# Kernel tuning notes

Hardware: AMD Instinct MI355X
Metric: run time of the kernel (lower is better)

Reference implementation:

```python
import jax, jax.numpy as jnp
import numpy as np

H = 16      # attention_head_num
DH = 64     # attention_head_size
D = H * DH  # out_dim = 1024


def setup_inputs() -> dict:
    key = jax.random.key(0)
    ks = jax.random.split(key, 9)
    s = 1.0 / np.sqrt(D)
    x = jax.random.normal(ks[0], (2, 2048, D), dtype=jnp.float32)
    Wq = jax.random.uniform(ks[1], (D, D), jnp.float32, -s, s)
    bq = jax.random.uniform(ks[2], (D,), jnp.float32, -s, s)
    Wk = jax.random.uniform(ks[3], (D, D), jnp.float32, -s, s)
    bk = jax.random.uniform(ks[4], (D,), jnp.float32, -s, s)
    Wv = jax.random.uniform(ks[5], (D, D), jnp.float32, -s, s)
    bv = jax.random.uniform(ks[6], (D,), jnp.float32, -s, s)
    Wo = jax.random.uniform(ks[7], (D, D), jnp.float32, -s, s)
    bo = jax.random.uniform(ks[8], (D,), jnp.float32, -s, s)
    return {"x": x, "Wq": Wq, "bq": bq, "Wk": Wk, "bk": bk,
            "Wv": Wv, "bv": bv, "Wo": Wo, "bo": bo}


def reference(x, Wq, bq, Wk, bk, Wv, bv, Wo, bo):
    B, S, _ = x.shape
    # projections (nn.Linear: x @ W^T + b)
    q = (x @ Wq.T + bq).reshape(B, S, H, DH).transpose(0, 2, 1, 3)  # [B,H,S,Dh]
    k = (x @ Wk.T + bk).reshape(B, S, H, DH).transpose(0, 2, 1, 3)
    v = (x @ Wv.T + bv).reshape(B, S, H, DH).transpose(0, 2, 1, 3)
    scores = jnp.einsum('bhqd,bhkd->bhqk', q, k) / jnp.sqrt(jnp.float32(DH))
    probs = jax.nn.softmax(scores, axis=-1)  # dropout is identity in eval mode
    ctx = jnp.einsum('bhqk,bhkd->bhqd', probs, v)
    ctx = ctx.transpose(0, 2, 1, 3).reshape(B, S, D)
    return ctx @ Wo.T + bo
```

## Files before the change

### kernel.cpp

```cpp
#include <hip/hip_runtime.h>
#include <hip/hip_bf16.h>
#include <stdint.h>

typedef __attribute__((ext_vector_type(8))) short bf16x8;
typedef __attribute__((ext_vector_type(8))) unsigned short u16x8;
typedef __attribute__((ext_vector_type(4))) unsigned short u16x4;
typedef __attribute__((ext_vector_type(4))) float f32x4;

constexpr int NB  = 2;
constexpr int NS  = 2048;
constexpr int NH  = 16;
constexpr int NDH = 64;
constexpr int ND  = 1024;

static __device__ __forceinline__ unsigned short bfbits(float f) {
    union { float f; uint32_t u; } v; v.f = f;
    uint32_t u = v.u + 0x7FFFu + ((v.u >> 16) & 1u);
    return (unsigned short)(u >> 16);
}

static __device__ __forceinline__ float fexp2(float x) {
#if __has_builtin(__builtin_amdgcn_exp2f)
    return __builtin_amdgcn_exp2f(x);
#else
    return exp2f(x);
#endif
}

static __device__ __forceinline__ void gl_lds16(const void* g, void* l) {
    __builtin_amdgcn_global_load_lds(
        (const __attribute__((address_space(1))) unsigned int*)g,
        (__attribute__((address_space(3))) unsigned int*)l, 16, 0, 0);
}

__global__ __launch_bounds__(256)
void cvt_kernel(const float* __restrict__ x,  const float* __restrict__ wq,
                const float* __restrict__ wk, const float* __restrict__ wv,
                const float* __restrict__ wo,
                unsigned short* __restrict__ xb,  unsigned short* __restrict__ wqb,
                unsigned short* __restrict__ wkb, unsigned short* __restrict__ wvb,
                unsigned short* __restrict__ wob)
{
    const int b = blockIdx.x;
    const float* s; unsigned short* d; int off;
    if      (b < 2048) { s = x;  d = xb;  off = b; }
    else if (b < 2560) { s = wq; d = wqb; off = b - 2048; }
    else if (b < 3072) { s = wk; d = wkb; off = b - 2560; }
    else if (b < 3584) { s = wv; d = wvb; off = b - 3072; }
    else               { s = wo; d = wob; off = b - 3584; }
    const size_t idx = ((size_t)off * 256 + threadIdx.x) * 8;
    float4 f0 = *(const float4*)&s[idx];
    float4 f1 = *(const float4*)&s[idx + 4];
    u16x8 o;
    o[0] = bfbits(f0.x); o[1] = bfbits(f0.y); o[2] = bfbits(f0.z); o[3] = bfbits(f0.w);
    o[4] = bfbits(f1.x); o[5] = bfbits(f1.y); o[6] = bfbits(f1.z); o[7] = bfbits(f1.w);
    *(u16x8*)&d[idx] = o;
}

__global__ __launch_bounds__(256, 2)
void qkv_kernel(const unsigned short* __restrict__ xb,
                const unsigned short* __restrict__ wqb,
                const unsigned short* __restrict__ wkb,
                const unsigned short* __restrict__ wvb,
                const float* __restrict__ bq, const float* __restrict__ bk,
                const float* __restrict__ bv,
                unsigned short* __restrict__ qbuf,
                unsigned short* __restrict__ kbuf,
                unsigned short* __restrict__ vtbuf)
{
    __shared__ unsigned short As[128 * 64];
    __shared__ unsigned short Bs[128 * 64];
    __shared__ unsigned short Tt[128][136];

    const int fid = blockIdx.x + blockIdx.y * 24;
    const int xcd = fid & 7, idx = fid >> 3;
    const int bx  = idx >> 2;
    const int by  = xcd * 4 + (idx & 3);

    const int m0  = by * 128;
    const int jg0 = bx * 128;
    const int proj = jg0 >> 10;
    const int n0   = jg0 & 1023;
    const unsigned short* W = (proj == 0) ? wqb : (proj == 1) ? wkb : wvb;
    const float* bias       = (proj == 0) ? bq  : (proj == 1) ? bk  : bv;

    const int tid = threadIdx.x, lane = tid & 63, wid = tid >> 6;
    const int wm = wid >> 1, wn = wid & 1;
    const int l15 = lane & 15, g = lane >> 4;

    const f32x4 fzero = {0.f, 0.f, 0.f, 0.f};
    f32x4 acc[4][4];
#pragma unroll
    for (int i = 0; i < 4; i++)
#pragma unroll
        for (int j = 0; j < 4; j++) acc[i][j] = fzero;

    const int srow = tid >> 3;
    const int scb  = ((tid & 7) * 16) ^ ((srow & 7) << 4);
    const char* asrc = (const char*)xb + (size_t)(m0 + srow) * 2048 + scb;
    const char* bsrc = (const char*)W  + (size_t)(n0 + srow) * 2048 + scb;
    char* adst = (char*)As + tid * 16;
    char* bdst = (char*)Bs + tid * 16;
    const int xm = (l15 & 7) << 4;

    for (int k0 = 0; k0 < 1024; k0 += 64) {
#pragma unroll
        for (int i = 0; i < 4; i++) {
            gl_lds16(asrc + (size_t)i * 32 * 2048 + k0 * 2, adst + i * 4096);
            gl_lds16(bsrc + (size_t)i * 32 * 2048 + k0 * 2, bdst + i * 4096);
        }
        __syncthreads();
#pragma unroll
        for (int kk = 0; kk < 2; kk++) {
            bf16x8 af[4], bfr[4];
#pragma unroll
            for (int i = 0; i < 4; i++) {
                const int row = wm * 64 + i * 16 + l15;
                af[i] = *(const bf16x8*)((const char*)As + row * 128 + ((kk * 64 + g * 16) ^ xm));
            }
#pragma unroll
            for (int j = 0; j < 4; j++) {
                const int row = wn * 64 + j * 16 + l15;
                bfr[j] = *(const bf16x8*)((const char*)Bs + row * 128 + ((kk * 64 + g * 16) ^ xm));
            }
#pragma unroll
            for (int i = 0; i < 4; i++)
#pragma unroll
                for (int j = 0; j < 4; j++)
                    acc[i][j] = __builtin_amdgcn_mfma_f32_16x16x32_bf16(af[i], bfr[j], acc[i][j], 0, 0, 0);
        }
        __syncthreads();
    }

    if (proj < 2) {
        unsigned short* qk_out = (proj == 0) ? qbuf : kbuf;
        const float qs = (proj == 0) ? 0.18033688f : 1.0f;
#pragma unroll
        for (int j = 0; j < 4; j++) {
            const int col = n0 + wn * 64 + j * 16 + l15;
            const float bsv = bias[col];
            const int h = col >> 6, dh = col & 63;
#pragma unroll
            for (int i = 0; i < 4; i++)
#pragma unroll
                for (int r = 0; r < 4; r++) {
                    const int row = m0 + wm * 64 + i * 16 + g * 4 + r;
                    const int b_ = row >> 11, s_ = row & (NS - 1);
                    qk_out[((size_t)((b_ * NH + h) * NS + s_)) * NDH + dh] =
                        bfbits((acc[i][j][r] + bsv) * qs);
                }
        }
    } else {
#pragma unroll
        for (int j = 0; j < 4; j++) {
            const int cl = wn * 64 + j * 16 + l15;
            const float bsv = bias[n0 + cl];
#pragma unroll
            for (int i = 0; i < 4; i++) {
                u16x4 w4;
#pragma unroll
                for (int r = 0; r < 4; r++) w4[r] = bfbits(acc[i][j][r] + bsv);
                *(u16x4*)&Tt[cl][wm * 64 + i * 16 + g * 4] = w4;
            }
        }
        __syncthreads();
        const int b_ = m0 >> 11, s0 = m0 & (NS - 1);
        const int h0 = n0 >> 6;
#pragma unroll
        for (int it = 0; it < 8; it++) {
            const int c = wid * 32 + it * 4 + g;
            u16x8 v8 = *(const u16x8*)&Tt[c][l15 * 8];
            const size_t row = (size_t)(b_ * NH + h0 + (c >> 6)) * NDH + (c & 63);
            *(u16x8*)&vtbuf[row * NS + s0 + l15 * 8] = v8;
        }
    }
}

__global__ __launch_bounds__(512, 6)
void attn_kernel(const unsigned short* __restrict__ qbuf,
                 const unsigned short* __restrict__ kbuf,
                 const unsigned short* __restrict__ vtbuf,
                 unsigned short* __restrict__ ctxbuf)
{
    __shared__ unsigned short Ks[3][64 * 64];
    __shared__ unsigned short Vs[3][64 * 64];

    const int fid  = blockIdx.x + blockIdx.y * 16;
    const int nid  = (fid % 8) * 64 + fid / 8;
    const int bx   = nid % 16, bh = nid / 16;
    const int q0   = bx * 128;

    const int tid = threadIdx.x, lane = tid & 63, wid = tid >> 6;
    const int l15 = lane & 15, g = lane >> 4;

    const unsigned short* qb = qbuf  + (size_t)bh * NS * NDH;
    const unsigned short* kb = kbuf  + (size_t)bh * NS * NDH;
    const unsigned short* vb = vtbuf + (size_t)bh * NDH * NS;

    const int qrow = q0 + wid * 16 + l15;
    const bf16x8 qf0 = *(const bf16x8*)&qb[(size_t)qrow * NDH + g * 8];
    const bf16x8 qf1 = *(const bf16x8*)&qb[(size_t)qrow * NDH + 32 + g * 8];

    const short oneb = (short)0x3F80;
    const bf16x8 ones = {oneb, oneb, oneb, oneb, oneb, oneb, oneb, oneb};

    const f32x4 fzero = {0.f, 0.f, 0.f, 0.f};
    f32x4 acc[4];
#pragma unroll
    for (int d = 0; d < 4; d++) acc[d] = fzero;
    f32x4 acc_l = fzero;

    const int o = tid * 16;
    const int srow = o >> 7;
    const int scb  = (o & 127) ^ ((srow & 7) << 4);
    const char* ksrc = (const char*)kb + srow * 128 + scb;
    const char* vsrc = (const char*)vb + (size_t)srow * (NS * 2) + scb;
    char* kbase = (char*)Ks;
    char* vbase = (char*)Vs;
    const int xm = (l15 & 7) << 4;

    auto STAGE = [&](int b, int t_) {
        gl_lds16(ksrc + (size_t)t_ * 8192, kbase + b * 8192 + o);
        gl_lds16(vsrc + (size_t)t_ * 128,  vbase + b * 8192 + o);
    };

    STAGE(0, 0);
    STAGE(1, 1);

    for (int t = 0; t < 32; t++) {
        if (t < 31) asm volatile("s_waitcnt vmcnt(2)" ::: "memory");
        else        asm volatile("s_waitcnt vmcnt(0)" ::: "memory");
        __builtin_amdgcn_s_barrier();
        asm volatile("" ::: "memory");
        if (t < 30) STAGE((t + 2) % 3, t + 2);

        const char* ksb = kbase + (t % 3) * 8192;
        const char* vsb = vbase + (t % 3) * 8192;

        f32x4 sv[4];
        __builtin_amdgcn_s_setprio(1);
#pragma unroll
        for (int kt = 0; kt < 4; kt++) {
            const char* rb = ksb + (kt * 16 + l15) * 128;
            bf16x8 kf0 = *(const bf16x8*)(rb + ((g * 16) ^ xm));
            bf16x8 kf1 = *(const bf16x8*)(rb + ((64 + g * 16) ^ xm));
            f32x4 s4 = fzero;
            s4 = __builtin_amdgcn_mfma_f32_16x16x32_bf16(kf0, qf0, s4, 0, 0, 0);
            s4 = __builtin_amdgcn_mfma_f32_16x16x32_bf16(kf1, qf1, s4, 0, 0, 0);
            sv[kt] = s4;
        }
        __builtin_amdgcn_s_setprio(0);

#pragma unroll
        for (int kt = 0; kt < 4; kt++)
#pragma unroll
            for (int r = 0; r < 4; r++)
                sv[kt][r] = fexp2(sv[kt][r]);

        bf16x8 pf[2];
#pragma unroll
        for (int f = 0; f < 2; f++) {
            const int kt0 = f * 2;
            union { __hip_bfloat162 h2; uint32_t u; } c0, c1, c2, c3;
            float2 p01 = { sv[kt0][0], sv[kt0][1] };
            float2 p23 = { sv[kt0][2], sv[kt0][3] };
            float2 p45 = { sv[kt0 + 1][0], sv[kt0 + 1][1] };
            float2 p67 = { sv[kt0 + 1][2], sv[kt0 + 1][3] };
            c0.h2 = __float22bfloat162_rn(p01);
            c1.h2 = __float22bfloat162_rn(p23);
            c2.h2 = __float22bfloat162_rn(p45);
            c3.h2 = __float22bfloat162_rn(p67);
            uint32_t a0 = c0.u, a1 = c1.u, b0 = c2.u, b1 = c3.u;
            asm("v_permlane32_swap_b32 %0, %1" : "+v"(a0), "+v"(b0));
            asm("v_permlane32_swap_b32 %0, %1" : "+v"(a1), "+v"(b1));
            asm("v_permlane16_swap_b32 %0, %1" : "+v"(a0), "+v"(b0));
            asm("v_permlane16_swap_b32 %0, %1" : "+v"(a1), "+v"(b1));
            union { uint32_t w[4]; bf16x8 fr; } r_;
            r_.w[0] = a0; r_.w[1] = a1; r_.w[2] = b0; r_.w[3] = b1;
            pf[f] = r_.fr;
        }

        __builtin_amdgcn_s_setprio(1);
        acc_l = __builtin_amdgcn_mfma_f32_16x16x32_bf16(pf[0], ones, acc_l, 0, 0, 0);
        acc_l = __builtin_amdgcn_mfma_f32_16x16x32_bf16(pf[1], ones, acc_l, 0, 0, 0);
#pragma unroll
        for (int d = 0; d < 4; d++) {
            const char* rb = vsb + (d * 16 + l15) * 128;
            bf16x8 vf0 = *(const bf16x8*)(rb + ((g * 16) ^ xm));
            bf16x8 vf1 = *(const bf16x8*)(rb + ((64 + g * 16) ^ xm));
            acc[d] = __builtin_amdgcn_mfma_f32_16x16x32_bf16(pf[0], vf0, acc[d], 0, 0, 0);
            acc[d] = __builtin_amdgcn_mfma_f32_16x16x32_bf16(pf[1], vf1, acc[d], 0, 0, 0);
        }
        __builtin_amdgcn_s_setprio(0);
    }

    const int b_ = bh >> 4, h_ = bh & 15;
#pragma unroll
    for (int r = 0; r < 4; r++) {
        const float inv = 1.f / acc_l[r];
        const int sq = q0 + wid * 16 + g * 4 + r;
        const size_t base = ((size_t)(b_ * NS + sq)) * ND + h_ * NDH;
#pragma unroll
        for (int d = 0; d < 4; d++)
            ctxbuf[base + d * 16 + l15] = bfbits(acc[d][r] * inv);
    }
}

__global__ __launch_bounds__(256, 2)
void out_kernel(const unsigned short* __restrict__ ctx,
                const unsigned short* __restrict__ wob,
                const float* __restrict__ bo,
                float* __restrict__ out)
{
    __shared__ unsigned short As[128 * 64];
    __shared__ unsigned short Bs[128 * 64];

    const int n0 = blockIdx.x * 128;
    const int m0 = blockIdx.y * 128;
    const int tid = threadIdx.x, lane = tid & 63, wid = tid >> 6;
    const int wm = wid >> 1, wn = wid & 1;
    const int l15 = lane & 15, g = lane >> 4;

    const f32x4 fzero = {0.f, 0.f, 0.f, 0.f};
    f32x4 acc[4][4];
#pragma unroll
    for (int i = 0; i < 4; i++)
#pragma unroll
        for (int j = 0; j < 4; j++) acc[i][j] = fzero;

    const int srow = tid >> 3;
    const int scb  = ((tid & 7) * 16) ^ ((srow & 7) << 4);
    const char* asrc = (const char*)ctx + (size_t)(m0 + srow) * 2048 + scb;
    const char* bsrc = (const char*)wob + (size_t)(n0 + srow) * 2048 + scb;
    char* adst = (char*)As + tid * 16;
    char* bdst = (char*)Bs + tid * 16;
    const int xm = (l15 & 7) << 4;

    for (int k0 = 0; k0 < 1024; k0 += 64) {
#pragma unroll
        for (int i = 0; i < 4; i++) {
            gl_lds16(asrc + (size_t)i * 32 * 2048 + k0 * 2, adst + i * 4096);
            gl_lds16(bsrc + (size_t)i * 32 * 2048 + k0 * 2, bdst + i * 4096);
        }
        __syncthreads();
#pragma unroll
        for (int kk = 0; kk < 2; kk++) {
            bf16x8 af[4], bfr[4];
#pragma unroll
            for (int i = 0; i < 4; i++) {
                const int row = wm * 64 + i * 16 + l15;
                af[i] = *(const bf16x8*)((const char*)As + row * 128 + ((kk * 64 + g * 16) ^ xm));
            }
#pragma unroll
            for (int j = 0; j < 4; j++) {
                const int row = wn * 64 + j * 16 + l15;
                bfr[j] = *(const bf16x8*)((const char*)Bs + row * 128 + ((kk * 64 + g * 16) ^ xm));
            }
#pragma unroll
            for (int i = 0; i < 4; i++)
#pragma unroll
                for (int j = 0; j < 4; j++)
                    acc[i][j] = __builtin_amdgcn_mfma_f32_16x16x32_bf16(af[i], bfr[j], acc[i][j], 0, 0, 0);
        }
        __syncthreads();
    }

#pragma unroll
    for (int j = 0; j < 4; j++) {
        const int col = n0 + wn * 64 + j * 16 + l15;
        const float bsv = bo[col];
#pragma unroll
        for (int i = 0; i < 4; i++)
#pragma unroll
            for (int r = 0; r < 4; r++) {
                const int row = m0 + wm * 64 + i * 16 + g * 4 + r;
                out[(size_t)row * ND + col] = acc[i][j][r] + bsv;
            }
    }
}

extern "C" void kernel_launch(void* const* d_in, const int* in_sizes, int n_in,
                              void* d_out, int out_size, void* d_ws, size_t ws_size,
                              hipStream_t stream) {
    const float* x  = (const float*)d_in[0];
    const float* Wq = (const float*)d_in[1];
    const float* bq = (const float*)d_in[2];
    const float* Wk = (const float*)d_in[3];
    const float* bk = (const float*)d_in[4];
    const float* Wv = (const float*)d_in[5];
    const float* bv = (const float*)d_in[6];
    const float* Wo = (const float*)d_in[7];
    const float* bo = (const float*)d_in[8];
    float* out = (float*)d_out;

    const size_t qk_elems = (size_t)NB * NH * NS * NDH;
    const size_t w_elems  = (size_t)ND * ND;
    unsigned short* qbuf   = (unsigned short*)d_ws;
    unsigned short* kbuf   = qbuf + qk_elems;
    unsigned short* vtbuf  = kbuf + qk_elems;
    unsigned short* ctxbuf = vtbuf + qk_elems;
    unsigned short* xb     = ctxbuf + qk_elems;
    unsigned short* wqb    = xb + qk_elems;
    unsigned short* wkb    = wqb + w_elems;
    unsigned short* wvb    = wkb + w_elems;
    unsigned short* wob    = wvb + w_elems;

    cvt_kernel<<<4096, 256, 0, stream>>>(x, Wq, Wk, Wv, Wo, xb, wqb, wkb, wvb, wob);
    qkv_kernel<<<dim3(24, 32), 256, 0, stream>>>(xb, wqb, wkb, wvb, bq, bk, bv,
                                                 qbuf, kbuf, vtbuf);
    attn_kernel<<<dim3(16, 32), 512, 0, stream>>>(qbuf, kbuf, vtbuf, ctxbuf);
    out_kernel<<<dim3(8, 32), 256, 0, stream>>>(ctxbuf, wob, bo, out);
}
```

Baseline: 115.2 us.

## Software-pipeline QK of next tile with softmax/PV of current tile in attention

Restructures the attention inner loop so the QK^T MFMAs for tile t+1 are issued alongside the exp/convert/PV work for tile t, using two score register sets. LDS staging grows from a 3-deep to a 4-deep ring so loads for t+3 can be in flight while two tiles are live. Occupancy hint drops from 6 to 4 blocks per SM to make room for the extra registers and shared memory. The aim is to hide MFMA and exp latency through instruction overlap, at the cost of fewer resident waves.

```diff
diff --git a/kernel.cpp b/kernel.cpp
--- a/kernel.cpp
+++ b/kernel.cpp
@@ -176,14 +176,14 @@
     }
 }
 
-__global__ __launch_bounds__(512, 6)
+__global__ __launch_bounds__(512, 4)
 void attn_kernel(const unsigned short* __restrict__ qbuf,
                  const unsigned short* __restrict__ kbuf,
                  const unsigned short* __restrict__ vtbuf,
                  unsigned short* __restrict__ ctxbuf)
 {
-    __shared__ unsigned short Ks[3][64 * 64];
-    __shared__ unsigned short Vs[3][64 * 64];
+    __shared__ unsigned short Ks[4][64 * 64];
+    __shared__ unsigned short Vs[4][64 * 64];
 
     const int fid  = blockIdx.x + blockIdx.y * 16;
     const int nid  = (fid % 8) * 64 + fid / 8;
@@ -224,20 +224,8 @@
         gl_lds16(vsrc + (size_t)t_ * 128,  vbase + b * 8192 + o);
     };
 
-    STAGE(0, 0);
-    STAGE(1, 1);
-
-    for (int t = 0; t < 32; t++) {
-        if (t < 31) asm volatile("s_waitcnt vmcnt(2)" ::: "memory");
-        else        asm volatile("s_waitcnt vmcnt(0)" ::: "memory");
-        __builtin_amdgcn_s_barrier();
-        asm volatile("" ::: "memory");
-        if (t < 30) STAGE((t + 2) % 3, t + 2);
-
-        const char* ksb = kbase + (t % 3) * 8192;
-        const char* vsb = vbase + (t % 3) * 8192;
-
-        f32x4 sv[4];
+    auto QK = [&](int h, f32x4 (&sv)[4]) {
+        const char* ksb = kbase + (h & 3) * 8192;
         __builtin_amdgcn_s_setprio(1);
 #pragma unroll
         for (int kt = 0; kt < 4; kt++) {
@@ -250,7 +238,10 @@
             sv[kt] = s4;
         }
         __builtin_amdgcn_s_setprio(0);
-
+    };
+
+    auto SMPV = [&](int h, f32x4 (&sv)[4]) {
+        const char* vsb = vbase + (h & 3) * 8192;
 #pragma unroll
         for (int kt = 0; kt < 4; kt++)
 #pragma unroll
@@ -292,7 +283,37 @@
             acc[d] = __builtin_amdgcn_mfma_f32_16x16x32_bf16(pf[1], vf1, acc[d], 0, 0, 0);
         }
         __builtin_amdgcn_s_setprio(0);
-    }
+    };
+
+    f32x4 svA[4], svB[4];
+
+    STAGE(0, 0); STAGE(1, 1); STAGE(2, 2);
+    asm volatile("s_waitcnt vmcnt(4)" ::: "memory");
+    __builtin_amdgcn_s_barrier();
+    asm volatile("" ::: "memory");
+    QK(0, svA);
+
+    for (int t = 0; t < 30; t += 2) {
+        asm volatile("s_waitcnt vmcnt(2)" ::: "memory");
+        __builtin_amdgcn_s_barrier();
+        asm volatile("" ::: "memory");
+        STAGE((t + 3) & 3, t + 3);
+        QK(t + 1, svB);
+        SMPV(t, svA);
+
+        asm volatile("s_waitcnt vmcnt(2)" ::: "memory");
+        __builtin_amdgcn_s_barrier();
+        asm volatile("" ::: "memory");
+        if (t + 4 < 32) STAGE((t + 4) & 3, t + 4);
+        QK(t + 2, svA);
+        SMPV(t + 1, svB);
+    }
+    asm volatile("s_waitcnt vmcnt(0)" ::: "memory");
+    __builtin_amdgcn_s_barrier();
+    asm volatile("" ::: "memory");
+    QK(31, svB);
+    SMPV(30, svA);
+    SMPV(31, svB);
 
     const int b_ = bh >> 4, h_ = bh & 15;
 #pragma unroll
```

Measured after the change: 115.6 us. Within noise of the previous version (+0.3%).
